# Optimization experiments

Measured on AMD Instinct MI355X. Metric: run time of the kernel, lower is better.

## Reference

```python
import jax, jax.numpy as jnp
import numpy as np

STD = 1.0  # components_std from cfg
LOG_2PI = float(np.log(2.0 * np.pi))


def setup_inputs() -> dict:
    key = jax.random.key(0)
    k1, k2, k3 = jax.random.split(key, 3)
    B, S, D, K = 256, 1024, 32, 512
    x = jax.random.normal(k1, (B, S, D), dtype=jnp.float32)
    logits = jax.random.normal(k2, (B, K), dtype=jnp.float32)
    # xavier_normal_ init on (K, D): std = sqrt(2 / (K + D))
    means = jax.random.normal(k3, (K, D), dtype=jnp.float32) * np.sqrt(2.0 / (K + D))
    return {"x": x, "logits": logits, "means": means}


def reference(x, logits, means):
    # x: [B, S, D], logits: [B, K], means: [K, D]
    D = x.shape[-1]
    log_mix = jax.nn.log_softmax(logits, axis=-1)  # [B, K] Categorical log-probs
    # squared distance ||x - mu||^2 via expansion (avoids [B,S,K,D] intermediate)
    x2 = jnp.sum(x * x, axis=-1)          # [B, S]
    m2 = jnp.sum(means * means, axis=-1)  # [K]
    xm = jnp.einsum('bsd,kd->bsk', x, means)  # [B, S, K]
    sq = x2[..., None] - 2.0 * xm + m2        # [B, S, K]
    inv_var = 1.0 / (STD * STD)
    log_norm = D * (jnp.log(jnp.float32(STD)) + 0.5 * LOG_2PI)
    comp_logpdf = -0.5 * inv_var * sq - log_norm  # [B, S, K] Independent-Normal logpdf
    # mixture log_prob = logsumexp over components; NLL = negative
    nll = -jax.nn.logsumexp(log_mix[:, None, :] + comp_logpdf, axis=-1)  # [B, S]
    return nll
```

## Files before the change

kernel.cpp:

```cpp
#include <hip/hip_runtime.h>
#include <math.h>

constexpr int Bc = 256, Sc = 1024, Dc = 32, Kc = 512;
constexpr int ST = 128;
constexpr float LOG2E    = 1.4426950408889634f;
constexpr float LN2      = 0.6931471805599453f;
constexpr float LOG_NORM = 29.40603306051f;

typedef __attribute__((ext_vector_type(4))) float f32x4;

#if __has_builtin(__builtin_amdgcn_exp2f)
#define EXP2F(v) __builtin_amdgcn_exp2f(v)
#else
#define EXP2F(v) exp2f(v)
#endif
#if __has_builtin(__builtin_amdgcn_logf)
#define LOG2F(v) __builtin_amdgcn_logf(v)
#else
#define LOG2F(v) log2f(v)
#endif

template <bool HI>
__device__ __forceinline__ int pkfp8(float a, float b, int old) {
    return __builtin_amdgcn_cvt_pk_fp8_f32(a, b, old, HI);
}

__device__ __forceinline__ int swz8(int row, int chunk) {
    return row * 32 + ((chunk ^ ((row >> 2) & 3)) << 3);
}

__global__ __launch_bounds__(256)
void gm_m2f8(const float* __restrict__ means,
             unsigned short* __restrict__ mf8, float* __restrict__ m2buf)
{
    const int t  = blockIdx.x * 256 + threadIdx.x;
    const float v0 = means[2 * t];
    const float v1 = means[2 * t + 1];
    mf8[t] = (unsigned short)(pkfp8<false>(v0, v1, 0) & 0xffff);
    float sq = v0 * v0 + v1 * v1;
    #pragma unroll
    for (int off = 1; off <= 8; off <<= 1) sq += __shfl_xor(sq, off);
    if ((threadIdx.x & 15) == 0) m2buf[t >> 4] = sq;
}

__global__ __launch_bounds__(512, 4)
void gm_main(const float* __restrict__ x, const float* __restrict__ logits,
             const float* __restrict__ m2buf, const unsigned short* __restrict__ mf8,
             float* __restrict__ out)
{
    __shared__ unsigned char mlds[Kc * 32];
    __shared__ float wlds[Kc];
    __shared__ float x2p[ST];
    __shared__ float red[16];

    const int tid  = threadIdx.x;
    const int lane = tid & 63;
    const int wid  = tid >> 6;
    const int b    = blockIdx.x >> 3;
    const int s0   = (blockIdx.x & 7) * ST;
    const int q    = lane >> 4;
    const int ln   = lane & 15;
    const int rw   = wid * 16;

    {
        const unsigned long long* src = (const unsigned long long*)mf8;
        #pragma unroll
        for (int j = 0; j < 4; ++j) {
            const int c = tid + j * 512;
            *(unsigned long long*)&mlds[swz8(c >> 2, c & 3)] = src[c];
        }
    }

    const float l = logits[b * Kc + tid];
    wlds[tid] = EXP2F((l - 0.5f * m2buf[tid]) * LOG2E);

    float mx = l;
    #pragma unroll
    for (int off = 32; off >= 1; off >>= 1) mx = fmaxf(mx, __shfl_xor(mx, off));
    if (lane == 0) red[wid] = mx;

    const int row = rw + ln;
    long a;
    {
        const float4* xp = (const float4*)(x + ((size_t)b * Sc + s0 + row) * Dc) + q * 2;
        float4 v0 = xp[0], v1 = xp[1];
        int2 A;
        A.x = pkfp8<false>(v0.x * LOG2E, v0.y * LOG2E, 0);
        A.x = pkfp8<true >(v0.z * LOG2E, v0.w * LOG2E, A.x);
        A.y = pkfp8<false>(v1.x * LOG2E, v1.y * LOG2E, 0);
        A.y = pkfp8<true >(v1.z * LOG2E, v1.w * LOG2E, A.y);
        a = *(const long*)&A;
        float p = v0.x*v0.x + v0.y*v0.y + v0.z*v0.z + v0.w*v0.w
                + v1.x*v1.x + v1.y*v1.y + v1.z*v1.z + v1.w*v1.w;
        p += __shfl_xor(p, 16); p += __shfl_xor(p, 32);
        if (q == 0) x2p[row] = p;
    }
    __syncthreads();

    const float mxb = fmaxf(fmaxf(fmaxf(red[0], red[1]), fmaxf(red[2], red[3])),
                            fmaxf(fmaxf(red[4], red[5]), fmaxf(red[6], red[7])));
    float sm = EXP2F((l - mxb) * LOG2E);
    #pragma unroll
    for (int off = 32; off >= 1; off >>= 1) sm += __shfl_xor(sm, off);
    if (lane == 0) red[8 + wid] = sm;

    const int bbase = ln * 32 + ((q ^ ((ln >> 2) & 3)) << 3);
    const f32x4 zero = {0.f, 0.f, 0.f, 0.f};
    float acc[4] = {0.f, 0.f, 0.f, 0.f};

    #pragma unroll 4
    for (int kt = 0; kt < 32; ++kt) {
        const long  bfr = *(const long*)&mlds[bbase + kt * 512];
        const float wv  = wlds[kt * 16 + ln];
        f32x4 d = __builtin_amdgcn_mfma_f32_16x16x32_fp8_fp8(a, bfr, zero, 0, 0, 0);
        #pragma unroll
        for (int r = 0; r < 4; ++r)
            acc[r] = fmaf(wv, EXP2F(d[r]), acc[r]);
    }
    __syncthreads();
    const float lse  = mxb + LN2 * LOG2F(((red[8]  + red[9])  + (red[10] + red[11]))
                                       + ((red[12] + red[13]) + (red[14] + red[15])));
    const float base = LOG_NORM + lse;

    #pragma unroll
    for (int r = 0; r < 4; ++r) {
        float s = acc[r];
        s += __shfl_xor(s, 1); s += __shfl_xor(s, 2);
        s += __shfl_xor(s, 4); s += __shfl_xor(s, 8);
        if (ln == 0) {
            const int r0 = rw + q * 4 + r;
            out[(size_t)b * Sc + s0 + r0] = 0.5f * x2p[r0] + base - LN2 * LOG2F(s);
        }
    }
}

extern "C" void kernel_launch(void* const* d_in, const int* in_sizes, int n_in,
                              void* d_out, int out_size, void* d_ws, size_t ws_size,
                              hipStream_t stream) {
    const float* x      = (const float*)d_in[0];
    const float* logits = (const float*)d_in[1];
    const float* means  = (const float*)d_in[2];
    float* out = (float*)d_out;
    (void)in_sizes; (void)n_in; (void)out_size; (void)ws_size;

    unsigned short* mf8   = (unsigned short*)d_ws;
    float*          m2buf = (float*)((char*)d_ws + 16384);

    hipLaunchKernelGGL(gm_m2f8, dim3(32), dim3(256), 0, stream, means, mf8, m2buf);
    hipLaunchKernelGGL(gm_main, dim3(Bc * (Sc / ST)), dim3(512), 0, stream,
                       x, logits, m2buf, mf8, out);
}
```

Measured before the change: 91.18 us.

## Use 32x32 fp8 MFMA, bit-trick exp approximation, and larger sequence tiles

Each block now covers 256 sequence rows, and each wave handles 32 rows using the 32x32x16 fp8 MFMA instead of the 16x16x32 variant. The hardware exp2 in the inner loop is replaced by a Schraudolph-style trick: it scales the exponent into the float bit pattern, adds a precomputed bias that folds in the mixture weight, and converts the result to int. This removes transcendental work from the hot loop and halves the block count. In exchange it adds approximation error to the exponential, and the new LDS layout drops the bank-conflict swizzle.

```diff
diff --git a/kernel.cpp b/kernel.cpp
--- a/kernel.cpp
+++ b/kernel.cpp
@@ -2,12 +2,17 @@
 #include <math.h>
 
 constexpr int Bc = 256, Sc = 1024, Dc = 32, Kc = 512;
-constexpr int ST = 128;
+constexpr int ST = 256;
 constexpr float LOG2E    = 1.4426950408889634f;
 constexpr float LN2      = 0.6931471805599453f;
 constexpr float LOG_NORM = 29.40603306051f;
 
-typedef __attribute__((ext_vector_type(4))) float f32x4;
+constexpr float FE_SCALE = 8388608.0f;
+constexpr float FE_BIAS  = 1064992048.0f;
+
+typedef __attribute__((ext_vector_type(4)))  float f32x4;
+typedef __attribute__((ext_vector_type(16))) float f32x16;
+typedef __attribute__((ext_vector_type(2)))  long  longx2;
 
 #if __has_builtin(__builtin_amdgcn_exp2f)
 #define EXP2F(v) __builtin_amdgcn_exp2f(v)
@@ -23,10 +28,6 @@
 template <bool HI>
 __device__ __forceinline__ int pkfp8(float a, float b, int old) {
     return __builtin_amdgcn_cvt_pk_fp8_f32(a, b, old, HI);
-}
-
-__device__ __forceinline__ int swz8(int row, int chunk) {
-    return row * 32 + ((chunk ^ ((row >> 2) & 3)) << 3);
 }
 
 __global__ __launch_bounds__(256)
@@ -48,7 +49,7 @@
              const float* __restrict__ m2buf, const unsigned short* __restrict__ mf8,
              float* __restrict__ out)
 {
-    __shared__ unsigned char mlds[Kc * 32];
+    __shared__ __align__(16) unsigned char mlds[Kc * 32];
     __shared__ float wlds[Kc];
     __shared__ float x2p[ST];
     __shared__ float red[16];
@@ -56,44 +57,53 @@
     const int tid  = threadIdx.x;
     const int lane = tid & 63;
     const int wid  = tid >> 6;
-    const int b    = blockIdx.x >> 3;
-    const int s0   = (blockIdx.x & 7) * ST;
-    const int q    = lane >> 4;
-    const int ln   = lane & 15;
-    const int rw   = wid * 16;
+    const int b    = blockIdx.x >> 2;
+    const int s0   = (blockIdx.x & 3) * ST;
+    const int l5   = lane & 31;
+    const int hi   = lane >> 5;
+    const int rw   = wid * 32;
 
     {
         const unsigned long long* src = (const unsigned long long*)mf8;
         #pragma unroll
         for (int j = 0; j < 4; ++j) {
             const int c = tid + j * 512;
-            *(unsigned long long*)&mlds[swz8(c >> 2, c & 3)] = src[c];
+            const int k = c >> 2, o = c & 3;
+            *(unsigned long long*)&mlds[k * 32 + ((o & 1) << 4) + ((o & 2) << 2)]
+                = src[c];
         }
     }
 
     const float l = logits[b * Kc + tid];
-    wlds[tid] = EXP2F((l - 0.5f * m2buf[tid]) * LOG2E);
+    wlds[tid] = fmaf((l - 0.5f * m2buf[tid]) * LOG2E, FE_SCALE, FE_BIAS);
 
     float mx = l;
     #pragma unroll
     for (int off = 32; off >= 1; off >>= 1) mx = fmaxf(mx, __shfl_xor(mx, off));
     if (lane == 0) red[wid] = mx;
 
-    const int row = rw + ln;
-    long a;
+    long a0, a1;
     {
-        const float4* xp = (const float4*)(x + ((size_t)b * Sc + s0 + row) * Dc) + q * 2;
-        float4 v0 = xp[0], v1 = xp[1];
+        const float4* xp = (const float4*)(x + ((size_t)b * Sc + s0 + rw + l5) * Dc);
+        const float4 v0 = xp[2 * hi],     v1 = xp[2 * hi + 1];
+        const float4 u0 = xp[2 * hi + 4], u1 = xp[2 * hi + 5];
         int2 A;
         A.x = pkfp8<false>(v0.x * LOG2E, v0.y * LOG2E, 0);
         A.x = pkfp8<true >(v0.z * LOG2E, v0.w * LOG2E, A.x);
         A.y = pkfp8<false>(v1.x * LOG2E, v1.y * LOG2E, 0);
         A.y = pkfp8<true >(v1.z * LOG2E, v1.w * LOG2E, A.y);
-        a = *(const long*)&A;
+        a0 = *(const long*)&A;
+        A.x = pkfp8<false>(u0.x * LOG2E, u0.y * LOG2E, 0);
+        A.x = pkfp8<true >(u0.z * LOG2E, u0.w * LOG2E, A.x);
+        A.y = pkfp8<false>(u1.x * LOG2E, u1.y * LOG2E, 0);
+        A.y = pkfp8<true >(u1.z * LOG2E, u1.w * LOG2E, A.y);
+        a1 = *(const long*)&A;
         float p = v0.x*v0.x + v0.y*v0.y + v0.z*v0.z + v0.w*v0.w
-                + v1.x*v1.x + v1.y*v1.y + v1.z*v1.z + v1.w*v1.w;
-        p += __shfl_xor(p, 16); p += __shfl_xor(p, 32);
-        if (q == 0) x2p[row] = p;
+                + v1.x*v1.x + v1.y*v1.y + v1.z*v1.z + v1.w*v1.w
+                + u0.x*u0.x + u0.y*u0.y + u0.z*u0.z + u0.w*u0.w
+                + u1.x*u1.x + u1.y*u1.y + u1.z*u1.z + u1.w*u1.w;
+        p += __shfl_xor(p, 32);
+        if (hi == 0) x2p[rw + l5] = p;
     }
     __syncthreads();
 
@@ -104,18 +114,22 @@
     for (int off = 32; off >= 1; off >>= 1) sm += __shfl_xor(sm, off);
     if (lane == 0) red[8 + wid] = sm;
 
-    const int bbase = ln * 32 + ((q ^ ((ln >> 2) & 3)) << 3);
-    const f32x4 zero = {0.f, 0.f, 0.f, 0.f};
-    float acc[4] = {0.f, 0.f, 0.f, 0.f};
+    const int bb = l5 * 32 + hi * 16;
+    const f32x16 zero16 = {0.f,0.f,0.f,0.f, 0.f,0.f,0.f,0.f,
+                           0.f,0.f,0.f,0.f, 0.f,0.f,0.f,0.f};
+    float acc[16];
+    #pragma unroll
+    for (int r = 0; r < 16; ++r) acc[r] = 0.f;
 
-    #pragma unroll 4
-    for (int kt = 0; kt < 32; ++kt) {
-        const long  bfr = *(const long*)&mlds[bbase + kt * 512];
-        const float wv  = wlds[kt * 16 + ln];
-        f32x4 d = __builtin_amdgcn_mfma_f32_16x16x32_fp8_fp8(a, bfr, zero, 0, 0, 0);
+    #pragma unroll 2
+    for (int cg = 0; cg < 16; ++cg) {
+        const longx2 bp = *(const longx2*)&mlds[cg * 1024 + bb];
+        const float  wv = wlds[cg * 32 + l5];
+        f32x16 d = __builtin_amdgcn_mfma_f32_32x32x16_fp8_fp8(a0, bp.x, zero16, 0, 0, 0);
+        d        = __builtin_amdgcn_mfma_f32_32x32x16_fp8_fp8(a1, bp.y, d,      0, 0, 0);
         #pragma unroll
-        for (int r = 0; r < 4; ++r)
-            acc[r] = fmaf(wv, EXP2F(d[r]), acc[r]);
+        for (int r = 0; r < 16; ++r)
+            acc[r] += __int_as_float((int)fmaf(d[r], FE_SCALE, wv));
     }
     __syncthreads();
     const float lse  = mxb + LN2 * LOG2F(((red[8]  + red[9])  + (red[10] + red[11]))
@@ -123,13 +137,14 @@
     const float base = LOG_NORM + lse;
 
     #pragma unroll
-    for (int r = 0; r < 4; ++r) {
+    for (int r = 0; r < 16; ++r) {
         float s = acc[r];
-        s += __shfl_xor(s, 1); s += __shfl_xor(s, 2);
-        s += __shfl_xor(s, 4); s += __shfl_xor(s, 8);
-        if (ln == 0) {
-            const int r0 = rw + q * 4 + r;
-            out[(size_t)b * Sc + s0 + r0] = 0.5f * x2p[r0] + base - LN2 * LOG2F(s);
+        s += __shfl_xor(s, 1);  s += __shfl_xor(s, 2);
+        s += __shfl_xor(s, 4);  s += __shfl_xor(s, 8);
+        s += __shfl_xor(s, 16);
+        if (l5 == 0) {
+            const int row = rw + (r & 3) + 8 * (r >> 2) + 4 * hi;
+            out[(size_t)b * Sc + s0 + row] = 0.5f * x2p[row] + base - LN2 * LOG2F(s);
         }
     }
 }
```

Result: no change. 92.75 us (+1.7%).
